# Optimization experiments

Measured on AMD Instinct MI355X. Metric: run time of the kernel, lower is better.

Reference implementation:

```python
import jax, jax.numpy as jnp
import numpy as np

B, N, E = 4, 20000, 320000
DIN, DMID, DOUT = 64, 64, 32


def setup_inputs() -> dict:
    key = jax.random.key(0)
    ks = jax.random.split(key, 32)
    p = lambda k, shape: jax.random.normal(k, shape, dtype=jnp.float32) * 0.05
    inp = {
        "x": jax.random.normal(ks[0], (B, N, DIN), dtype=jnp.float32),
        "edge_index": jax.random.randint(ks[1], (2, E), 0, N, dtype=jnp.int32),
        "edge_weights": jax.random.uniform(ks[2], (E,), dtype=jnp.float32),
        "prev_hidden_state": jax.random.normal(ks[3], (B, N, DMID), dtype=jnp.float32),
        # GCNConv weights (lin bias=False, separate conv bias) for z/r/h gates
        "Wz": p(ks[4], (DIN, DMID)), "bz": jnp.zeros((DMID,), jnp.float32),
        "Wr": p(ks[5], (DIN, DMID)), "br": jnp.zeros((DMID,), jnp.float32),
        "Wh": p(ks[6], (DIN, DMID)), "bh": jnp.zeros((DMID,), jnp.float32),
        # GRU gate linears: Linear(2*dmid, dmid)
        "Lz": p(ks[7], (2 * DMID, DMID)), "lbz": jnp.zeros((DMID,), jnp.float32),
        "Lr": p(ks[8], (2 * DMID, DMID)), "lbr": jnp.zeros((DMID,), jnp.float32),
        "Lh": p(ks[9], (2 * DMID, DMID)), "lbh": jnp.zeros((DMID,), jnp.float32),
        # GlobalAttention gate_nn: Linear(dmid, 1)
        "gate_w": p(ks[10], (DMID, 1)), "gate_b": jnp.zeros((1,), jnp.float32),
        # head
        "W1": p(ks[11], (DMID, DMID)), "b1": jnp.zeros((DMID,), jnp.float32),
        "W2": p(ks[12], (DMID, DOUT)), "b2": jnp.zeros((DOUT,), jnp.float32),
    }
    return inp


def _gcn(X, W, b, src, dst, norm, n_nodes):
    # X: (B,N,din). GCNConv with add_self_loops=False: scatter(norm * (XW)[src]) + b
    xw = jnp.einsum("bnf,fd->bnd", X, W)              # (B,N,dmid)
    msg = xw[:, src, :] * norm[None, :, None]          # (B,E,dmid)
    agg = jnp.zeros_like(xw).at[:, dst, :].add(msg)    # (B,N,dmid)
    return agg + b


def reference(x, edge_index, edge_weights, prev_hidden_state,
              Wz, bz, Wr, br, Wh, bh,
              Lz, lbz, Lr, lbr, Lh, lbh,
              gate_w, gate_b, W1, b1, W2, b2):
    edge_index = edge_index.reshape(2, -1)
    edge_weights = edge_weights.reshape(-1)
    n_nodes = x.shape[1]
    src, dst = edge_index[0], edge_index[1]

    # symmetric gcn_norm (no self loops): D^-1/2 A D^-1/2
    deg = jnp.zeros((n_nodes,), x.dtype).at[dst].add(edge_weights)
    dinv = jnp.where(deg > 0, jax.lax.rsqrt(jnp.maximum(deg, 1e-12)), 0.0)
    norm = dinv[src] * edge_weights * dinv[dst]

    H = prev_hidden_state
    # TGCN2 GRU-style gates
    Z = jax.nn.sigmoid(jnp.concatenate([_gcn(x, Wz, bz, src, dst, norm, n_nodes), H], -1) @ Lz + lbz)
    R = jax.nn.sigmoid(jnp.concatenate([_gcn(x, Wr, br, src, dst, norm, n_nodes), H], -1) @ Lr + lbr)
    Ht = jnp.tanh(jnp.concatenate([_gcn(x, Wh, bh, src, dst, norm, n_nodes), H * R], -1) @ Lh + lbh)
    H_new = Z * H + (1.0 - Z) * Ht                     # (B,N,dmid)

    # GlobalAttention pooling over nodes per graph
    gate = H_new @ gate_w + gate_b                     # (B,N,1)
    attn = jax.nn.softmax(gate, axis=1)
    y = jnp.sum(attn * H_new, axis=1)                  # (B,dmid)

    y = jax.nn.relu(y @ W1 + b1)
    y = y @ W2 + b2                                    # (B,dout)
    return (y, H_new)
```

## Files before the change

### kernel.cpp

```cpp
#include <hip/hip_runtime.h>
#include <hip/hip_bf16.h>

typedef unsigned short u16;
typedef float f32x4 __attribute__((ext_vector_type(4)));
typedef short s16x8 __attribute__((ext_vector_type(8)));

#define NB 4
#define NN 20000
#define NE 320000
#define ROWS (NB*NN)
#define NBLK 313
#define SLOTCAP 64
#define XTBLK 5000
#define FSBLK 1250
#define AGGB 5000
#define PREPB 6

__device__ __forceinline__ float b2f(u16 u){
  union{unsigned int i; float f;} v; v.i = ((unsigned int)u)<<16; return v.f;
}
__device__ __forceinline__ u16 f2b(float f){
  __hip_bfloat16 h = __float2bfloat16(f);
  return __builtin_bit_cast(u16, h);
}

__global__ void __launch_bounds__(256, 8) setup_kernel(
    const float* __restrict__ x, ushort4* __restrict__ xt4,
    const int* __restrict__ ei, const float* __restrict__ ew,
    int* __restrict__ cursor, int2* __restrict__ slots){
  int bid = blockIdx.x;
  if(bid < FSBLK){
    int e = bid*256 + threadIdx.x;
    int s = ei[e], d = ei[NE + e];
    float w = ew[e];
    int p = atomicAdd(&cursor[d], 1);
    if(p < SLOTCAP){
      int2 ent; ent.x = s; ent.y = __float_as_int(w);
      slots[d*SLOTCAP + p] = ent;
    }
  } else {
    int t = (bid - FSBLK)*256 + threadIdx.x;
    int b = t / (NN*16);
    int rem = t - b*(NN*16);
    int n = rem >> 4;
    int c4 = rem & 15;
    float4 v = reinterpret_cast<const float4*>(x)[t];
    ushort4 o; o.x=f2b(v.x); o.y=f2b(v.y); o.z=f2b(v.z); o.w=f2b(v.w);
    xt4[(size_t)n*64 + b*16 + c4] = o;
  }
}

__device__ __forceinline__ float dinvf(float d){
  return (d > 0.f) ? rsqrtf(fmaxf(d, 1e-12f)) : 0.f;
}

__global__ void __launch_bounds__(256, 8) degsum_kernel(
    const int* __restrict__ cursor, const int2* __restrict__ slots,
    float* __restrict__ dinv){
  int node = (blockIdx.x*256 + threadIdx.x) >> 4;
  int sub  = threadIdx.x & 15;
  if(node >= NN) return;
  int cnt = min(cursor[node], SLOTCAP);
  const int2* sl = slots + (size_t)node*SLOTCAP;
  float s = 0.f;
  for(int j=sub; j<cnt; j+=16) s += __int_as_float(sl[j].y);
  s += __shfl_xor(s, 1, 16);
  s += __shfl_xor(s, 2, 16);
  s += __shfl_xor(s, 4, 16);
  s += __shfl_xor(s, 8, 16);
  if(sub == 0) dinv[node] = dinvf(s);
}

__global__ void agg_kernel(const ushort4* __restrict__ xt4, const float* __restrict__ dinv,
                           const int* __restrict__ cursor, const int2* __restrict__ slots,
                           u16* __restrict__ agg,
                           const float* Wz, const float* bz, const float* Lz, const float* lbz,
                           const float* Wr, const float* br, const float* Lr, const float* lbr,
                           const float* Wh, const float* bh, const float* Lh, const float* lbh,
                           int4* __restrict__ wfrag, float* __restrict__ cvec){
  __shared__ __align__(16) float Pl[4096];
  if(blockIdx.x >= AGGB){
    int m = blockIdx.x - AGGB;
    int g = m >> 1, half = m & 1;
    const float* W  = (g==0)?Wz:(g==1)?Wr:Wh;
    const float* L  = (g==0)?Lz:(g==1)?Lr:Lh;
    const float* bb = (g==0)?bz:(g==1)?br:bh;
    const float* lb = (g==0)?lbz:(g==1)?lbr:lbh;
    int t = threadIdx.x;
    if(half == 0){
      for(int i=t; i<1024; i+=256)
        reinterpret_cast<float4*>(Pl)[i] = reinterpret_cast<const float4*>(L)[i];
      __syncthreads();
      int i = t >> 2, j0 = (t & 3) * 16;
      float acc[16];
      #pragma unroll
      for(int q=0;q<16;q++) acc[q] = 0.f;
      for(int kb=0; kb<16; kb++){
        float4 w4 = *reinterpret_cast<const float4*>(W + i*64 + kb*4);
        const float* l0 = Pl + (kb*4)*64 + j0;
        #pragma unroll
        for(int q=0;q<16;q++) acc[q] += w4.x * l0[q];
        #pragma unroll
        for(int q=0;q<16;q++) acc[q] += w4.y * l0[64+q];
        #pragma unroll
        for(int q=0;q<16;q++) acc[q] += w4.z * l0[128+q];
        #pragma unroll
        for(int q=0;q<16;q++) acc[q] += w4.w * l0[192+q];
      }
      float cv = 0.f;
      if(t < 64){
        cv = lb[t];
        for(int k=0;k<64;k++) cv += bb[k]*Pl[k*64+t];
      }
      __syncthreads();
      #pragma unroll
      for(int q=0;q<16;q++) Pl[i*64 + j0 + q] = acc[q];
      if(t < 64) cvec[g*64 + t] = cv;
      __syncthreads();
    } else {
      for(int i=t; i<1024; i+=256)
        reinterpret_cast<float4*>(Pl)[i] = reinterpret_cast<const float4*>(L + 4096)[i];
      __syncthreads();
    }
    for(int it=t; it<512; it+=256){
      int l  = it & 63;
      int rl = it >> 6;
      int s  = rl >> 2, tt = rl & 3;
      int k0 = s*32 + (l>>4)*8;
      int n  = tt*16 + (l&15);
      union { u16 v[8]; int4 q4; } tmp;
      #pragma unroll
      for(int j=0;j<8;j++) tmp.v[j] = f2b(Pl[(k0+j)*64 + n]);
      wfrag[m*512 + it] = tmp.q4;
    }
    return;
  }
  int wave = (blockIdx.x*blockDim.x + threadIdx.x) >> 6;
  int lane = threadIdx.x & 63;
  if(wave >= NN) return;
  int cnt = min(cursor[wave], SLOTCAP);
  float dn = dinv[wave];
  const int2* sl = slots + (size_t)wave*SLOTCAP;
  float a0=0.f, a1=0.f, a2=0.f, a3=0.f;
  int j = 0;
  for(; j+3 < cnt; j+=4){
    int2 ea = sl[j],   eb = sl[j+1];
    int2 ec = sl[j+2], ed = sl[j+3];
    ushort4 va = xt4[(size_t)ea.x*64 + lane];
    ushort4 vb = xt4[(size_t)eb.x*64 + lane];
    ushort4 vc = xt4[(size_t)ec.x*64 + lane];
    ushort4 vd = xt4[(size_t)ed.x*64 + lane];
    float wa = dinv[ea.x] * __int_as_float(ea.y) * dn;
    float wb = dinv[eb.x] * __int_as_float(eb.y) * dn;
    float wc = dinv[ec.x] * __int_as_float(ec.y) * dn;
    float wd = dinv[ed.x] * __int_as_float(ed.y) * dn;
    a0 += wa*b2f(va.x) + wb*b2f(vb.x) + wc*b2f(vc.x) + wd*b2f(vd.x);
    a1 += wa*b2f(va.y) + wb*b2f(vb.y) + wc*b2f(vc.y) + wd*b2f(vd.y);
    a2 += wa*b2f(va.z) + wb*b2f(vb.z) + wc*b2f(vc.z) + wd*b2f(vd.z);
    a3 += wa*b2f(va.w) + wb*b2f(vb.w) + wc*b2f(vc.w) + wd*b2f(vd.w);
  }
  for(; j < cnt; j++){
    int2 e = sl[j];
    float w = dinv[e.x] * __int_as_float(e.y) * dn;
    ushort4 v = xt4[(size_t)e.x*64 + lane];
    a0 += w * b2f(v.x);
    a1 += w * b2f(v.y);
    a2 += w * b2f(v.z);
    a3 += w * b2f(v.w);
  }
  int b = lane >> 4, c4 = lane & 15;
  ushort4 o; o.x=f2b(a0); o.y=f2b(a1); o.z=f2b(a2); o.w=f2b(a3);
  reinterpret_cast<ushort4*>(agg)[((size_t)b*NN + wave)*16 + c4] = o;
}

#define LDW(m,s,t) __builtin_bit_cast(s16x8, wfrag[((m)*8+(s)*4+(t))*64 + lane])

__global__ void __launch_bounds__(256, 4) gate_kernel(
    const u16* __restrict__ agg, const float* __restrict__ H,
    const int4* __restrict__ wfrag, const float* __restrict__ cvec,
    const float* __restrict__ gate_w, const float* __restrict__ gate_b,
    float* __restrict__ Hnew, float* __restrict__ ypart, float* __restrict__ dpart)
{
  __shared__ __align__(16) u16 rlds[4][1152];
  __shared__ float ylds[4][64];
  __shared__ float dlds[4];

  const int warp = threadIdx.x >> 6, lane = threadIdx.x & 63;
  const int mrow = lane & 15, quad = lane >> 4;
  const int bat = blockIdx.x / NBLK;
  const int blk = blockIdx.x % NBLK;
  const int tin = blk*4 + warp;
  const bool valid = (tin < 1250);
  const int r0 = bat*NN + tin*16;

  float czv[4], crv[4], chv[4], gwv[4];
  #pragma unroll
  for(int t=0;t<4;t++){
    czv[t] = cvec[t*16+mrow];
    crv[t] = cvec[64 + t*16+mrow];
    chv[t] = cvec[128 + t*16+mrow];
    gwv[t] = gate_w[t*16+mrow];
  }
  const float gb = gate_b[0];

  f32x4 Zc[4], Rc[4], Hc[4];
  union { f32x4 v4[2]; float f[8]; } u0, u1;
  if(valid){
    const int4* ap = reinterpret_cast<const int4*>(agg + (size_t)(r0+mrow)*64);
    s16x8 a0 = __builtin_bit_cast(s16x8, ap[quad]);
    s16x8 a1 = __builtin_bit_cast(s16x8, ap[4+quad]);

    const float* Hrow = H + (size_t)(r0+mrow)*64;
    u0.v4[0] = *reinterpret_cast<const f32x4*>(Hrow + quad*8);
    u0.v4[1] = *reinterpret_cast<const f32x4*>(Hrow + quad*8 + 4);
    u1.v4[0] = *reinterpret_cast<const f32x4*>(Hrow + 32 + quad*8);
    u1.v4[1] = *reinterpret_cast<const f32x4*>(Hrow + 32 + quad*8 + 4);
    s16x8 h0, h1;
    #pragma unroll
    for(int j=0;j<8;j++){
      h0[j] = (short)f2b(u0.f[j]);
      h1[j] = (short)f2b(u1.f[j]);
    }

    #pragma unroll
    for(int t=0;t<4;t++){
      f32x4 acc = {0.f,0.f,0.f,0.f};
      acc = __builtin_amdgcn_mfma_f32_16x16x32_bf16(a0, LDW(0,0,t), acc, 0,0,0);
      acc = __builtin_amdgcn_mfma_f32_16x16x32_bf16(a1, LDW(0,1,t), acc, 0,0,0);
      acc = __builtin_amdgcn_mfma_f32_16x16x32_bf16(h0, LDW(1,0,t), acc, 0,0,0);
      acc = __builtin_amdgcn_mfma_f32_16x16x32_bf16(h1, LDW(1,1,t), acc, 0,0,0);
      Zc[t] = acc;
      f32x4 ar = {0.f,0.f,0.f,0.f};
      ar = __builtin_amdgcn_mfma_f32_16x16x32_bf16(a0, LDW(2,0,t), ar, 0,0,0);
      ar = __builtin_amdgcn_mfma_f32_16x16x32_bf16(a1, LDW(2,1,t), ar, 0,0,0);
      ar = __builtin_amdgcn_mfma_f32_16x16x32_bf16(h0, LDW(3,0,t), ar, 0,0,0);
      ar = __builtin_amdgcn_mfma_f32_16x16x32_bf16(h1, LDW(3,1,t), ar, 0,0,0);
      Rc[t] = ar;
      f32x4 ah = {0.f,0.f,0.f,0.f};
      ah = __builtin_amdgcn_mfma_f32_16x16x32_bf16(a0, LDW(4,0,t), ah, 0,0,0);
      ah = __builtin_amdgcn_mfma_f32_16x16x32_bf16(a1, LDW(4,1,t), ah, 0,0,0);
      Hc[t] = ah;
    }

    #pragma unroll
    for(int t=0;t<4;t++){
      #pragma unroll
      for(int i=0;i<4;i++){
        float r = 1.f/(1.f + __expf(-(Rc[t][i] + crv[t])));
        rlds[warp][(quad*4+i)*72 + t*16 + mrow] = f2b(r);
      }
    }
    const u16* rp = &rlds[warp][mrow*72 + quad*8];
    int4 rv0 = *reinterpret_cast<const int4*>(rp);
    int4 rv1 = *reinterpret_cast<const int4*>(rp + 32);
    const u16* rv0p = reinterpret_cast<const u16*>(&rv0);
    const u16* rv1p = reinterpret_cast<const u16*>(&rv1);
    s16x8 hr0, hr1;
    #pragma unroll
    for(int j=0;j<8;j++){
      hr0[j] = (short)f2b(u0.f[j] * b2f(rv0p[j]));
      hr1[j] = (short)f2b(u1.f[j] * b2f(rv1p[j]));
    }
    #pragma unroll
    for(int t=0;t<4;t++){
      Hc[t] = __builtin_amdgcn_mfma_f32_16x16x32_bf16(hr0, LDW(5,0,t), Hc[t], 0,0,0);
      Hc[t] = __builtin_amdgcn_mfma_f32_16x16x32_bf16(hr1, LDW(5,1,t), Hc[t], 0,0,0);
    }

    float hnv[4][4];
    float ga[4] = {0.f,0.f,0.f,0.f};
    #pragma unroll
    for(int t=0;t<4;t++){
      #pragma unroll
      for(int i=0;i<4;i++){
        int row = r0 + quad*4 + i, col = t*16 + mrow;
        float z  = 1.f/(1.f + __expf(-(Zc[t][i] + czv[t])));
        float ht = tanhf(Hc[t][i] + chv[t]);
        float hv = H[(size_t)row*64 + col];
        float hn = z*hv + (1.f - z)*ht;
        Hnew[(size_t)row*64 + col] = hn;
        hnv[t][i] = hn;
        ga[i] += hn * gwv[t];
      }
    }
    #pragma unroll
    for(int i=0;i<4;i++){
      float v = ga[i];
      v += __shfl_xor(v, 1, 64);
      v += __shfl_xor(v, 2, 64);
      v += __shfl_xor(v, 4, 64);
      v += __shfl_xor(v, 8, 64);
      ga[i] = v;
    }
    float e_[4]; float dsum = 0.f;
    #pragma unroll
    for(int i=0;i<4;i++){ e_[i] = __expf(ga[i] + gb); dsum += e_[i]; }
    #pragma unroll
    for(int t=0;t<4;t++){
      float s = 0.f;
      #pragma unroll
      for(int i=0;i<4;i++) s += e_[i]*hnv[t][i];
      s += __shfl_xor(s, 16, 64);
      s += __shfl_xor(s, 32, 64);
      if(lane < 16) ylds[warp][t*16 + mrow] = s;
    }
    dsum += __shfl_xor(dsum, 16, 64);
    dsum += __shfl_xor(dsum, 32, 64);
    if(lane == 0) dlds[warp] = dsum;
  } else {
    if(lane < 16){
      #pragma unroll
      for(int t=0;t<4;t++) ylds[warp][t*16 + mrow] = 0.f;
    }
    if(lane == 0) dlds[warp] = 0.f;
  }
  __syncthreads();
  int t = threadIdx.x;
  if(t < 64){
    float s = ylds[0][t] + ylds[1][t] + ylds[2][t] + ylds[3][t];
    ypart[(size_t)blockIdx.x*64 + t] = s;
  }
  if(t == 64) dpart[blockIdx.x] = dlds[0] + dlds[1] + dlds[2] + dlds[3];
}

__global__ void __launch_bounds__(256) head_kernel(
    const float* __restrict__ ypart, const float* __restrict__ dpart,
    const float* W1, const float* b1,
    const float* W2, const float* b2, float* out){
  __shared__ float red[4][64];
  __shared__ float yv[64];
  __shared__ float hid[64];
  __shared__ float dshared;
  int b = blockIdx.x, t = threadIdx.x;
  int d = t & 63, q = t >> 6;
  const float* yp = ypart + (size_t)b*NBLK*64;
  float s = 0.f;
  #pragma unroll 4
  for(int k=q; k<NBLK; k+=4) s += yp[k*64 + d];
  red[q][d] = s;
  if(t < 64){
    const float* dp = dpart + b*NBLK;
    float ds = 0.f;
    for(int k=t; k<NBLK; k+=64) ds += dp[k];
    ds += __shfl_xor(ds, 1, 64);
    ds += __shfl_xor(ds, 2, 64);
    ds += __shfl_xor(ds, 4, 64);
    ds += __shfl_xor(ds, 8, 64);
    ds += __shfl_xor(ds, 16, 64);
    ds += __shfl_xor(ds, 32, 64);
    if(t == 0) dshared = ds;
  }
  __syncthreads();
  if(t < 64) yv[t] = red[0][t] + red[1][t] + red[2][t] + red[3][t];
  __syncthreads();
  if(t < 64){
    float inv = 1.f / dshared;
    float acc = b1[t];
    #pragma unroll 4
    for(int k=0;k<64;k++) acc += (yv[k]*inv) * W1[k*64+t];
    hid[t] = fmaxf(acc, 0.f);
  }
  __syncthreads();
  if(t < 32){
    float a2 = b2[t];
    #pragma unroll 4
    for(int d2=0; d2<64; d2++) a2 += hid[d2] * W2[d2*32+t];
    out[b*32+t] = a2;
  }
}

extern "C" void kernel_launch(void* const* d_in, const int* in_sizes, int n_in,
                              void* d_out, int out_size, void* d_ws, size_t ws_size,
                              hipStream_t stream) {
  const float* x   = (const float*)d_in[0];
  const int*   ei  = (const int*)d_in[1];
  const float* ew  = (const float*)d_in[2];
  const float* H   = (const float*)d_in[3];
  const float* Wz = (const float*)d_in[4],  *bz = (const float*)d_in[5];
  const float* Wr = (const float*)d_in[6],  *br = (const float*)d_in[7];
  const float* Wh = (const float*)d_in[8],  *bh = (const float*)d_in[9];
  const float* Lz = (const float*)d_in[10], *lbz = (const float*)d_in[11];
  const float* Lr = (const float*)d_in[12], *lbr = (const float*)d_in[13];
  const float* Lh = (const float*)d_in[14], *lbh = (const float*)d_in[15];
  const float* gw = (const float*)d_in[16], *gbp = (const float*)d_in[17];
  const float* W1 = (const float*)d_in[18], *b1 = (const float*)d_in[19];
  const float* W2 = (const float*)d_in[20], *b2 = (const float*)d_in[21];

  float* y_out    = (float*)d_out;
  float* Hnew_out = (float*)d_out + 128;

  char* ws = (char*)d_ws;
  size_t off = 0;
  auto alloc = [&](size_t bytes)->char*{
    off = (off + 255) & ~(size_t)255;
    char* p = ws + off; off += bytes; return p;
  };
  float*   dinv     = (float*)alloc(NN*4);
  int*     cursor   = (int*)  alloc(NN*4);
  int2*    slots    = (int2*) alloc((size_t)NN*SLOTCAP*8);
  ushort4* xt4      = (ushort4*)alloc((size_t)NN*256*2);
  u16*     agg      = (u16*)  alloc((size_t)ROWS*64*2);
  int4*    wfrag    = (int4*) alloc(3072*16);
  float*   cvec     = (float*)alloc(192*4);
  float*   ypart    = (float*)alloc((size_t)NB*NBLK*64*4);
  float*   dpart    = (float*)alloc((size_t)NB*NBLK*4);
  (void)ws_size; (void)n_in; (void)in_sizes; (void)out_size;

  hipMemsetAsync(cursor, 0, NN*4, stream);

  setup_kernel<<<FSBLK + XTBLK, 256, 0, stream>>>(
      x, xt4, ei, ew, cursor, slots);
  degsum_kernel<<<FSBLK, 256, 0, stream>>>(cursor, slots, dinv);
  agg_kernel<<<AGGB + PREPB, 256, 0, stream>>>(
      xt4, dinv, cursor, slots, agg,
      Wz,bz,Lz,lbz, Wr,br,Lr,lbr, Wh,bh,Lh,lbh, wfrag, cvec);
  gate_kernel<<<NB*NBLK, 256, 0, stream>>>(agg, H, wfrag, cvec, gw, gbp, Hnew_out, ypart, dpart);
  head_kernel<<<4, 256, 0, stream>>>(ypart, dpart, W1, b1, W2, b2, y_out);
}
```

Baseline: 216.6 us.

## Fuse head into gate kernel via last-block atomic reduction and fast activations

```diff
diff --git a/kernel.cpp b/kernel.cpp
--- a/kernel.cpp
+++ b/kernel.cpp
@@ -22,6 +22,13 @@
 __device__ __forceinline__ u16 f2b(float f){
   __hip_bfloat16 h = __float2bfloat16(f);
   return __builtin_bit_cast(u16, h);
+}
+
+__device__ __forceinline__ float fsig(float x){
+  return __builtin_amdgcn_rcpf(1.f + __expf(-x));
+}
+__device__ __forceinline__ float ftanh(float x){
+  return 1.f - 2.f*__builtin_amdgcn_rcpf(__expf(2.f*x) + 1.f);
 }
 
 __global__ void __launch_bounds__(256, 8) setup_kernel(
@@ -179,11 +186,18 @@
     const u16* __restrict__ agg, const float* __restrict__ H,
     const int4* __restrict__ wfrag, const float* __restrict__ cvec,
     const float* __restrict__ gate_w, const float* __restrict__ gate_b,
-    float* __restrict__ Hnew, float* __restrict__ ypart, float* __restrict__ dpart)
+    float* __restrict__ Hnew,
+    float* __restrict__ yacc, float* __restrict__ dacc, unsigned int* __restrict__ done,
+    const float* __restrict__ W1, const float* __restrict__ b1,
+    const float* __restrict__ W2, const float* __restrict__ b2,
+    float* __restrict__ out)
 {
   __shared__ __align__(16) u16 rlds[4][1152];
   __shared__ float ylds[4][64];
   __shared__ float dlds[4];
+  __shared__ int lastflag;
+  __shared__ float yv_s[4][64];
+  __shared__ float hid_s[4][64];
 
   const int warp = threadIdx.x >> 6, lane = threadIdx.x & 63;
   const int mrow = lane & 15, quad = lane >> 4;
@@ -246,7 +260,7 @@
     for(int t=0;t<4;t++){
       #pragma unroll
       for(int i=0;i<4;i++){
-        float r = 1.f/(1.f + __expf(-(Rc[t][i] + crv[t])));
+        float r = fsig(Rc[t][i] + crv[t]);
         rlds[warp][(quad*4+i)*72 + t*16 + mrow] = f2b(r);
       }
     }
@@ -274,8 +288,8 @@
       #pragma unroll
       for(int i=0;i<4;i++){
         int row = r0 + quad*4 + i, col = t*16 + mrow;
-        float z  = 1.f/(1.f + __expf(-(Zc[t][i] + czv[t])));
-        float ht = tanhf(Hc[t][i] + chv[t]);
+        float z  = fsig(Zc[t][i] + czv[t]);
+        float ht = ftanh(Hc[t][i] + chv[t]);
         float hv = H[(size_t)row*64 + col];
         float hn = z*hv + (1.f - z)*ht;
         Hnew[(size_t)row*64 + col] = hn;
@@ -318,54 +332,35 @@
   int t = threadIdx.x;
   if(t < 64){
     float s = ylds[0][t] + ylds[1][t] + ylds[2][t] + ylds[3][t];
-    ypart[(size_t)blockIdx.x*64 + t] = s;
-  }
-  if(t == 64) dpart[blockIdx.x] = dlds[0] + dlds[1] + dlds[2] + dlds[3];
-}
-
-__global__ void __launch_bounds__(256) head_kernel(
-    const float* __restrict__ ypart, const float* __restrict__ dpart,
-    const float* W1, const float* b1,
-    const float* W2, const float* b2, float* out){
-  __shared__ float red[4][64];
-  __shared__ float yv[64];
-  __shared__ float hid[64];
-  __shared__ float dshared;
-  int b = blockIdx.x, t = threadIdx.x;
-  int d = t & 63, q = t >> 6;
-  const float* yp = ypart + (size_t)b*NBLK*64;
-  float s = 0.f;
-  #pragma unroll 4
-  for(int k=q; k<NBLK; k+=4) s += yp[k*64 + d];
-  red[q][d] = s;
-  if(t < 64){
-    const float* dp = dpart + b*NBLK;
-    float ds = 0.f;
-    for(int k=t; k<NBLK; k+=64) ds += dp[k];
-    ds += __shfl_xor(ds, 1, 64);
-    ds += __shfl_xor(ds, 2, 64);
-    ds += __shfl_xor(ds, 4, 64);
-    ds += __shfl_xor(ds, 8, 64);
-    ds += __shfl_xor(ds, 16, 64);
-    ds += __shfl_xor(ds, 32, 64);
-    if(t == 0) dshared = ds;
-  }
+    atomicAdd(&yacc[bat*64 + t], s);
+  }
+  if(t == 64) atomicAdd(&dacc[bat], dlds[0] + dlds[1] + dlds[2] + dlds[3]);
   __syncthreads();
-  if(t < 64) yv[t] = red[0][t] + red[1][t] + red[2][t] + red[3][t];
+  if(t == 0){
+    __threadfence();
+    unsigned int old = atomicAdd(done, 1u);
+    lastflag = (old == (unsigned int)(NB*NBLK - 1));
+  }
   __syncthreads();
-  if(t < 64){
-    float inv = 1.f / dshared;
-    float acc = b1[t];
+  if(lastflag){
+    __threadfence();
+    int b = t >> 6, dcol = t & 63;
+    float dv   = __hip_atomic_load(&dacc[b], __ATOMIC_RELAXED, __HIP_MEMORY_SCOPE_AGENT);
+    float yval = __hip_atomic_load(&yacc[b*64 + dcol], __ATOMIC_RELAXED, __HIP_MEMORY_SCOPE_AGENT);
+    yv_s[b][dcol] = yval / dv;
+    __syncthreads();
+    float acc = b1[dcol];
     #pragma unroll 4
-    for(int k=0;k<64;k++) acc += (yv[k]*inv) * W1[k*64+t];
-    hid[t] = fmaxf(acc, 0.f);
-  }
-  __syncthreads();
-  if(t < 32){
-    float a2 = b2[t];
-    #pragma unroll 4
-    for(int d2=0; d2<64; d2++) a2 += hid[d2] * W2[d2*32+t];
-    out[b*32+t] = a2;
+    for(int k=0;k<64;k++) acc += yv_s[b][k] * W1[k*64 + dcol];
+    hid_s[b][dcol] = fmaxf(acc, 0.f);
+    __syncthreads();
+    if(t < 128){
+      int bb = t >> 5, c = t & 31;
+      float a2 = b2[c];
+      #pragma unroll 4
+      for(int d2=0; d2<64; d2++) a2 += hid_s[bb][d2] * W2[d2*32 + c];
+      out[bb*32 + c] = a2;
+    }
   }
 }
 
@@ -395,18 +390,20 @@
     off = (off + 255) & ~(size_t)255;
     char* p = ws + off; off += bytes; return p;
   };
+  char*    zr       = alloc(NN*4 + 2048);
+  int*     cursor   = (int*)zr;
+  float*   yacc     = (float*)(zr + NN*4);
+  float*   dacc     = (float*)(zr + NN*4 + 1024);
+  unsigned int* done= (unsigned int*)(zr + NN*4 + 1024 + 16);
   float*   dinv     = (float*)alloc(NN*4);
-  int*     cursor   = (int*)  alloc(NN*4);
   int2*    slots    = (int2*) alloc((size_t)NN*SLOTCAP*8);
   ushort4* xt4      = (ushort4*)alloc((size_t)NN*256*2);
   u16*     agg      = (u16*)  alloc((size_t)ROWS*64*2);
   int4*    wfrag    = (int4*) alloc(3072*16);
   float*   cvec     = (float*)alloc(192*4);
-  float*   ypart    = (float*)alloc((size_t)NB*NBLK*64*4);
-  float*   dpart    = (float*)alloc((size_t)NB*NBLK*4);
   (void)ws_size; (void)n_in; (void)in_sizes; (void)out_size;
 
-  hipMemsetAsync(cursor, 0, NN*4, stream);
+  hipMemsetAsync(zr, 0, NN*4 + 1024 + 16 + 4, stream);
 
   setup_kernel<<<FSBLK + XTBLK, 256, 0, stream>>>(
       x, xt4, ei, ew, cursor, slots);
@@ -414,6 +411,7 @@
   agg_kernel<<<AGGB + PREPB, 256, 0, stream>>>(
       xt4, dinv, cursor, slots, agg,
       Wz,bz,Lz,lbz, Wr,br,Lr,lbr, Wh,bh,Lh,lbh, wfrag, cvec);
-  gate_kernel<<<NB*NBLK, 256, 0, stream>>>(agg, H, wfrag, cvec, gw, gbp, Hnew_out, ypart, dpart);
-  head_kernel<<<4, 256, 0, stream>>>(ypart, dpart, W1, b1, W2, b2, y_out);
-}
+  gate_kernel<<<NB*NBLK, 256, 0, stream>>>(
+      agg, H, wfrag, cvec, gw, gbp, Hnew_out,
+      yacc, dacc, done, W1, b1, W2, b2, y_out);
+}
```

After: 251.6 us. 1.16x slower.
